# Performance work log

Measured on AMD Instinct MI355X. Metric: run time of the kernel, lower is better.

The kernel has to match this reference:

```python
import jax, jax.numpy as jnp
import numpy as np

N_NODES = 50000
NEG_SLOPE = 0.2


def setup_inputs() -> dict:
    key = jax.random.key(0)
    k1, k2, k3, k4, k5 = jax.random.split(key, 5)
    in_c, out_c = 256, 256
    n_edges = 1_600_000
    x = jax.random.normal(k1, (N_NODES, in_c), dtype=jnp.float32)
    edge_index = jax.random.randint(k2, (2, n_edges), 0, N_NODES, dtype=jnp.int64)
    # Glorot-ish scaled params
    W = jax.random.normal(k3, (in_c, out_c), dtype=jnp.float32) * (1.0 / np.sqrt(in_c))
    att_src = jax.random.normal(k4, (out_c,), dtype=jnp.float32) * (1.0 / np.sqrt(out_c))
    att_dst = jax.random.normal(k5, (out_c,), dtype=jnp.float32) * (1.0 / np.sqrt(out_c))
    bias = jnp.zeros((out_c,), dtype=jnp.float32)
    return {"x": x, "edge_index": edge_index, "W": W, "att_src": att_src, "att_dst": att_dst, "bias": bias}


def reference(x, edge_index, W, att_src, att_dst, bias):
    N = x.shape[0]
    # PyG GATConv default: add self loops
    loops = jnp.arange(N, dtype=edge_index.dtype)
    src = jnp.concatenate([edge_index[0], loops])  # [E+N]
    dst = jnp.concatenate([edge_index[1], loops])  # [E+N]

    h = x @ W  # [N, out_c]
    a_s = h @ att_src  # [N] per-node source attention term
    a_d = h @ att_dst  # [N] per-node destination attention term

    e = a_s[src] + a_d[dst]  # [E+N]
    e = jnp.where(e > 0, e, NEG_SLOPE * e)  # LeakyReLU(0.2)

    # scatter-softmax over edges sharing a destination node
    e_max = jax.ops.segment_max(e, dst, num_segments=N)  # [N]
    e_exp = jnp.exp(e - e_max[dst])  # [E+N]
    denom = jax.ops.segment_sum(e_exp, dst, num_segments=N)  # [N]
    alpha = e_exp / denom[dst]  # [E+N]

    msgs = alpha[:, None] * h[src]  # [E+N, out_c]
    out = jax.ops.segment_sum(msgs, dst, num_segments=N)  # [N, out_c]
    return out + bias
```

## Files before the change

kernel.cpp:

```cpp
#include <hip/hip_runtime.h>
#include <math.h>

#define NODES_C 256
#define NEG_SLOPE 0.2f
#define CAP 128

typedef __attribute__((ext_vector_type(8))) short short8;
typedef __attribute__((ext_vector_type(4))) float f32x4;
typedef __attribute__((ext_vector_type(2))) float f32x2;

__device__ inline unsigned short f2bf(float f) {
    unsigned u = __float_as_uint(f);
    u = (u + 0x7fff + ((u >> 16) & 1)) >> 16;
    return (unsigned short)u;
}
__device__ inline unsigned cvtpk_bf16(float a, float b) {
    unsigned r;
    asm("v_cvt_pk_bf16_f32 %0, %1, %2" : "=v"(r) : "v"(a), "v"(b));
    return r;
}
__device__ inline void gload_lds16(const void* g, void* l) {
    __builtin_amdgcn_global_load_lds(
        (const __attribute__((address_space(1))) unsigned int*)g,
        (__attribute__((address_space(3))) unsigned int*)l, 16, 0, 0);
}
__device__ inline void fma2(f32x2& a, unsigned u, float w) {
    f32x2 h;
    h.x = __uint_as_float(u << 16);
    h.y = __uint_as_float(u & 0xffff0000u);
    a += h * w;
}

__global__ __launch_bounds__(256) void k_init(const float* __restrict__ W,
                                              unsigned short* __restrict__ wt,
                                              uint4* __restrict__ zbase,
                                              int nZero4, int nbZero) {
    const int tid = threadIdx.x;
    int bid = blockIdx.x;
    if (bid < nbZero) {
        const int base = bid * 1024 + tid;
#pragma unroll
        for (int k = 0; k < 4; ++k) {
            const int i = base + k * 256;
            if (i < nZero4) zbase[i] = make_uint4(0, 0, 0, 0);
        }
        return;
    }
    bid -= nbZero;
    const int base = bid * 1024 + tid;
#pragma unroll
    for (int k = 0; k < 4; ++k) {
        const int i = base + k * 256;
        wt[i] = f2bf(W[(i & 255) * NODES_C + (i >> 8)]);
    }
}

__global__ __launch_bounds__(256) void k_stageB(
    const float* __restrict__ x, const unsigned short* __restrict__ wt,
    const float* __restrict__ att_src, const float* __restrict__ att_dst,
    unsigned short* __restrict__ hb, float* __restrict__ a_s, float* __restrict__ a_d,
    int n) {
    __shared__ unsigned short Ab[128 * 32];
    __shared__ unsigned short Bb[128 * 32];
    __shared__ float pfs[2][128], pfd[2][128];
    const int tid = threadIdx.x;
    const int lane = tid & 63;
    const int wid = tid >> 6;

    const int gbid = blockIdx.x;
    const int wr = wid >> 1, wc = wid & 1;
    const int brow = (gbid >> 1) * 128;
    const int bcol = (gbid & 1) * 128;
    const int rsel = lane & 15, ksel = (lane >> 4) * 8;

    f32x4 acc[4][4] = {};
    const int c0 = wid, c1 = wid + 4;
    const int srow0 = c0 * 16 + (lane >> 2), srow1 = c1 * 16 + (lane >> 2);
    const int sk = (lane & 3) * 8;
    const int arow = tid >> 1;
    const int kh = (tid & 1) * 16;
    const float4* xsrc = (const float4*)(x + (size_t)min(brow + arow, n - 1) * NODES_C);
    uint4* adst = (uint4*)&Ab[arow * 32 + kh];

    for (int kk = 0; kk < 256; kk += 32) {
        const int kb = (kk + kh) >> 2;
        const float4 v0 = xsrc[kb + 0];
        const float4 v1 = xsrc[kb + 1];
        const float4 v2 = xsrc[kb + 2];
        const float4 v3 = xsrc[kb + 3];
        gload_lds16(wt + (size_t)(bcol + srow0) * NODES_C + kk + sk, Bb + c0 * 512);
        gload_lds16(wt + (size_t)(bcol + srow1) * NODES_C + kk + sk, Bb + c1 * 512);
        adst[0] = make_uint4(cvtpk_bf16(v0.x, v0.y), cvtpk_bf16(v0.z, v0.w),
                             cvtpk_bf16(v1.x, v1.y), cvtpk_bf16(v1.z, v1.w));
        adst[1] = make_uint4(cvtpk_bf16(v2.x, v2.y), cvtpk_bf16(v2.z, v2.w),
                             cvtpk_bf16(v3.x, v3.y), cvtpk_bf16(v3.z, v3.w));
        __syncthreads();
        short8 afrag[4], bfrag[4];
#pragma unroll
        for (int m = 0; m < 4; ++m)
            afrag[m] = *(const short8*)&Ab[(wr * 64 + m * 16 + rsel) * 32 + ksel];
#pragma unroll
        for (int q = 0; q < 4; ++q)
            bfrag[q] = *(const short8*)&Bb[(wc * 64 + q * 16 + rsel) * 32 + ksel];
#pragma unroll
        for (int m = 0; m < 4; ++m)
#pragma unroll
            for (int q = 0; q < 4; ++q)
                acc[m][q] = __builtin_amdgcn_mfma_f32_16x16x32_bf16(bfrag[q], afrag[m], acc[m][q], 0, 0, 0);
        __syncthreads();
    }

    const int xr = lane & 15;
    const int cg = (lane >> 4) * 4;
    float4 avs4[4], avd4[4];
#pragma unroll
    for (int q = 0; q < 4; ++q) {
        avs4[q] = *(const float4*)&att_src[bcol + wc * 64 + q * 16 + cg];
        avd4[q] = *(const float4*)&att_dst[bcol + wc * 64 + q * 16 + cg];
    }
#pragma unroll
    for (int m = 0; m < 4; ++m) {
        const int rloc = wr * 64 + m * 16 + xr;
        const int r = brow + rloc;
        float s = 0.f, d = 0.f;
#pragma unroll
        for (int q = 0; q < 4; ++q) {
            const f32x4 v = acc[m][q];
            s += v[0] * avs4[q].x + v[1] * avs4[q].y + v[2] * avs4[q].z + v[3] * avs4[q].w;
            d += v[0] * avd4[q].x + v[1] * avd4[q].y + v[2] * avd4[q].z + v[3] * avd4[q].w;
            if (r < n) {
                const uint2 hv = make_uint2(cvtpk_bf16(v[0], v[1]), cvtpk_bf16(v[2], v[3]));
                *(uint2*)&hb[(size_t)r * NODES_C + bcol + wc * 64 + q * 16 + cg] = hv;
            }
        }
        s += __shfl_xor(s, 16); s += __shfl_xor(s, 32);
        d += __shfl_xor(d, 16); d += __shfl_xor(d, 32);
        if (lane < 16) { pfs[wc][rloc] = s; pfd[wc][rloc] = d; }
    }
    __syncthreads();
    if (tid < 128) {
        const int r = brow + tid;
        if (r < n) atomicAdd(&a_s[r], pfs[0][tid] + pfs[1][tid]);
    } else {
        const int t2 = tid - 128;
        const int r = brow + t2;
        if (r < n) atomicAdd(&a_d[r], pfd[0][t2] + pfd[1][t2]);
    }
}

__global__ __launch_bounds__(256) void k_permute(const int* __restrict__ src,
                                                 const int* __restrict__ dst,
                                                 const float* __restrict__ a_s,
                                                 const float* __restrict__ a_d,
                                                 int* __restrict__ cnt,
                                                 unsigned* __restrict__ sedge, int E2) {
    const int i = blockIdx.x * blockDim.x + threadIdx.x;
    if (i >= E2) return;
    const int2 sv = ((const int2*)src)[i];
    const int2 dv = ((const int2*)dst)[i];
#pragma unroll
    for (int k = 0; k < 2; ++k) {
        const int s = k ? sv.y : sv.x;
        const int d = k ? dv.y : dv.x;
        float e = a_s[s] + a_d[d];
        e = e > 0.f ? e : NEG_SLOPE * e;
        const float w = __expf(e);
        const int pos = atomicAdd(&cnt[d], 1);
        if (pos < CAP) sedge[(d << 7) + pos] = ((unsigned)f2bf(w) << 16) | (unsigned)s;
    }
}

__global__ __launch_bounds__(256) void k_gather(const int* __restrict__ cnt,
                                                const unsigned* __restrict__ sedge,
                                                const unsigned short* __restrict__ hb,
                                                const float* __restrict__ a_s,
                                                const float* __restrict__ a_d,
                                                const float* __restrict__ bias,
                                                float* __restrict__ out, int n) {
    const int node = (int)((blockIdx.x * (size_t)blockDim.x + threadIdx.x) >> 6);
    const int lane = threadIdx.x & 63;
    if (node >= n) return;
    const int c = __builtin_amdgcn_readfirstlane(cnt[node]);
    const int base = node << 7;
    const int hf = lane >> 5, q = lane & 31;
    const uint4* hrow = (const uint4*)hb;

    float eself = a_s[node] + a_d[node];
    eself = eself > 0.f ? eself : NEG_SLOPE * eself;
    const unsigned selfmeta = ((unsigned)f2bf(__expf(eself)) << 16) | (unsigned)node;
    const int items = c + 1;

    f32x2 acc0 = {0.f, 0.f}, acc1 = {0.f, 0.f}, acc2 = {0.f, 0.f}, acc3 = {0.f, 0.f};
    float dsum = 0.f;

    int it = 0;
    for (; it + 16 <= c; it += 16) {
        const int bi = __builtin_amdgcn_readfirstlane(base + it);
        unsigned p[16];
#pragma unroll
        for (int k = 0; k < 16; ++k) p[k] = sedge[bi + k];
        uint4 r[8];
#pragma unroll
        for (int k = 0; k < 8; ++k) {
            const unsigned m = hf ? p[2 * k + 1] : p[2 * k];
            r[k] = hrow[(size_t)(m & 0xffffu) * 32 + q];
        }
#pragma unroll
        for (int k = 0; k < 8; ++k) {
            const unsigned m = hf ? p[2 * k + 1] : p[2 * k];
            const float w = __uint_as_float(m & 0xffff0000u);
            dsum += w;
            fma2(acc0, r[k].x, w); fma2(acc1, r[k].y, w);
            fma2(acc2, r[k].z, w); fma2(acc3, r[k].w, w);
        }
    }
    for (; it < items; it += 2) {
        const int bi = __builtin_amdgcn_readfirstlane(base + it);
        const unsigned m0 = (it     < c) ? sedge[bi]     : ((it     == c) ? selfmeta : 0u);
        const unsigned m1 = (it + 1 < c) ? sedge[bi + 1] : ((it + 1 == c) ? selfmeta : 0u);
        const unsigned m = hf ? m1 : m0;
        const uint4 r = hrow[(size_t)(m & 0xffffu) * 32 + q];
        const float w = __uint_as_float(m & 0xffff0000u);
        dsum += w;
        fma2(acc0, r.x, w); fma2(acc1, r.y, w);
        fma2(acc2, r.z, w); fma2(acc3, r.w, w);
    }

    dsum += __shfl_xor(dsum, 32);
    acc0.x += __shfl_xor(acc0.x, 32); acc0.y += __shfl_xor(acc0.y, 32);
    acc1.x += __shfl_xor(acc1.x, 32); acc1.y += __shfl_xor(acc1.y, 32);
    acc2.x += __shfl_xor(acc2.x, 32); acc2.y += __shfl_xor(acc2.y, 32);
    acc3.x += __shfl_xor(acc3.x, 32); acc3.y += __shfl_xor(acc3.y, 32);

    const float inv = 1.f / dsum;
    const f32x2 A = hf ? acc2 : acc0;
    const f32x2 B = hf ? acc3 : acc1;
    const int ch = q * 8 + hf * 4;
    const float4 b4 = *(const float4*)&bias[ch];
    float4 o;
    o.x = fmaf(A.x, inv, b4.x);
    o.y = fmaf(A.y, inv, b4.y);
    o.z = fmaf(B.x, inv, b4.z);
    o.w = fmaf(B.y, inv, b4.w);
    *(float4*)&out[(size_t)node * NODES_C + ch] = o;
}

extern "C" void kernel_launch(void* const* d_in, const int* in_sizes, int n_in,
                              void* d_out, int out_size, void* d_ws, size_t ws_size,
                              hipStream_t stream) {
    const float* x       = (const float*)d_in[0];
    const int*   edge    = (const int*)d_in[1];
    const float* W       = (const float*)d_in[2];
    const float* att_src = (const float*)d_in[3];
    const float* att_dst = (const float*)d_in[4];
    const float* bias    = (const float*)d_in[5];
    float* out = (float*)d_out;

    const int n = in_sizes[0] / NODES_C;
    const int E = in_sizes[1] / 2;
    const int Mpad = (n + 127) & ~127;
    const int* src = edge;
    const int* dst = edge + E;

    char* p = (char*)d_ws;
    auto carve = [&p](size_t bytes) { char* r = p; p += (bytes + 255) & ~(size_t)255; return r; };
    unsigned short* wt = (unsigned short*)carve((size_t)NODES_C * NODES_C * 2);
    unsigned short* hb = (unsigned short*)carve((size_t)n * NODES_C * 2);
    float* a_s = (float*)carve((size_t)n * 4 * 3);
    float* a_d = a_s + n;
    int*   cnt = (int*)(a_d + n);
    unsigned* sedge = (unsigned*)carve((size_t)n * CAP * 4);

    const int nZero4 = (n * 3) / 4;
    const int nbZero = (nZero4 + 1023) / 1024;
    const int nbCvtw = (NODES_C * NODES_C) / 1024;

    k_init<<<nbZero + nbCvtw, 256, 0, stream>>>(W, wt, (uint4*)a_s, nZero4, nbZero);
    k_stageB<<<(Mpad / 128) * 2, 256, 0, stream>>>(
        x, wt, att_src, att_dst, hb, a_s, a_d, n);
    k_permute<<<(E / 2 + 255) / 256, 256, 0, stream>>>(src, dst, a_s, a_d, cnt, sedge, E / 2);
    k_gather<<<(n + 3) / 4, 256, 0, stream>>>(cnt, sedge, hb, a_s, a_d, bias, out, n);
}
```

Baseline: 261.9 us.

## Partition edge bucketing by destination slice to localize atomics and scatter writes

The edge permute kernel now launches NSLICE groups of blocks, each handling only edges whose destination falls in one node slice. Each slice rereads the whole dst array with nontemporal 16-byte loads and loads src only when a match is present. This is meant to keep the atomic counters and sedge scatter writes for a slice within a smaller working set that fits in cache, possibly XCD-local. The cost is reading dst eight times and relying on blockIdx-to-XCD mapping for locality.

```diff
diff --git a/kernel.cpp b/kernel.cpp
--- a/kernel.cpp
+++ b/kernel.cpp
@@ -4,10 +4,12 @@
 #define NODES_C 256
 #define NEG_SLOPE 0.2f
 #define CAP 128
+#define NSLICE 8
 
 typedef __attribute__((ext_vector_type(8))) short short8;
 typedef __attribute__((ext_vector_type(4))) float f32x4;
 typedef __attribute__((ext_vector_type(2))) float f32x2;
+typedef __attribute__((ext_vector_type(4))) int i32x4;
 
 __device__ inline unsigned short f2bf(float f) {
     unsigned u = __float_as_uint(f);
@@ -153,20 +155,36 @@
                                                  const float* __restrict__ a_s,
                                                  const float* __restrict__ a_d,
                                                  int* __restrict__ cnt,
-                                                 unsigned* __restrict__ sedge, int E2) {
-    const int i = blockIdx.x * blockDim.x + threadIdx.x;
-    if (i >= E2) return;
-    const int2 sv = ((const int2*)src)[i];
-    const int2 dv = ((const int2*)dst)[i];
-#pragma unroll
-    for (int k = 0; k < 2; ++k) {
-        const int s = k ? sv.y : sv.x;
-        const int d = k ? dv.y : dv.x;
-        float e = a_s[s] + a_d[d];
-        e = e > 0.f ? e : NEG_SLOPE * e;
-        const float w = __expf(e);
-        const int pos = atomicAdd(&cnt[d], 1);
-        if (pos < CAP) sedge[(d << 7) + pos] = ((unsigned)f2bf(w) << 16) | (unsigned)s;
+                                                 unsigned* __restrict__ sedge,
+                                                 int E4, int bps, int nsNode, int n) {
+    const int slice = blockIdx.x & (NSLICE - 1);
+    const int j = blockIdx.x >> 3;
+    const int lo = slice * nsNode;
+    const int hi = min(lo + nsNode, n);
+    const int stride = bps * 256;
+    const i32x4* d4 = (const i32x4*)dst;
+    const i32x4* s4 = (const i32x4*)src;
+
+    for (int g = j * 256 + threadIdx.x; g < E4; g += stride) {
+        const i32x4 dv = __builtin_nontemporal_load(&d4[g]);
+        const bool m0 = (dv.x >= lo) & (dv.x < hi);
+        const bool m1 = (dv.y >= lo) & (dv.y < hi);
+        const bool m2 = (dv.z >= lo) & (dv.z < hi);
+        const bool m3 = (dv.w >= lo) & (dv.w < hi);
+        if (!(m0 | m1 | m2 | m3)) continue;
+        const i32x4 sv = __builtin_nontemporal_load(&s4[g]);
+#pragma unroll
+        for (int k = 0; k < 4; ++k) {
+            const bool mk = k == 0 ? m0 : k == 1 ? m1 : k == 2 ? m2 : m3;
+            if (!mk) continue;
+            const int d = k == 0 ? dv.x : k == 1 ? dv.y : k == 2 ? dv.z : dv.w;
+            const int s = k == 0 ? sv.x : k == 1 ? sv.y : k == 2 ? sv.z : sv.w;
+            float e = a_s[s] + a_d[d];
+            e = e > 0.f ? e : NEG_SLOPE * e;
+            const float w = __expf(e);
+            const int pos = atomicAdd(&cnt[d], 1);
+            if (pos < CAP) sedge[(d << 7) + pos] = ((unsigned)f2bf(w) << 16) | (unsigned)s;
+        }
     }
 }
 
@@ -278,6 +296,11 @@
     k_init<<<nbZero + nbCvtw, 256, 0, stream>>>(W, wt, (uint4*)a_s, nZero4, nbZero);
     k_stageB<<<(Mpad / 128) * 2, 256, 0, stream>>>(
         x, wt, att_src, att_dst, hb, a_s, a_d, n);
-    k_permute<<<(E / 2 + 255) / 256, 256, 0, stream>>>(src, dst, a_s, a_d, cnt, sedge, E / 2);
+
+    const int E4 = E / 4;
+    const int bps = 192;
+    const int nsNode = (n + NSLICE - 1) / NSLICE;
+    k_permute<<<bps * NSLICE, 256, 0, stream>>>(src, dst, a_s, a_d, cnt, sedge,
+                                                E4, bps, nsNode, n);
     k_gather<<<(n + 3) / 4, 256, 0, stream>>>(cnt, sedge, hb, a_s, a_d, bias, out, n);
 }
```

New measurement: 236.7 us. 9.6% less time.
